# Kernel tuning notes

Hardware: AMD Instinct MI355X
Metric: run time of the kernel (lower is better)

Reference implementation:

```python
import jax, jax.numpy as jnp
import numpy as np

N, E, B = 50000, 800000, 64
ND, ED, HID, NC = 64, 16, 128, 6
HEADS = [4, 4, 1]
CH = [32, 32, 128]
CONCAT = [True, True, False]

PNAMES = ['pW', 'pb'] + [f'{p}{l}' for l in range(3) for p in ['W', 'as', 'ad', 'ae', 'We', 'b', 'g', 'be']] + ['gW1', 'gb1', 'gW2', 'gb2', 'cW1', 'cb1', 'cW2', 'cb2']


def _gat_conv(x, src, dst, ea, W, a_s, a_d, a_e, We, b, heads, ch, concat):
    n = x.shape[0]
    xp = (x @ W).reshape(n, heads, ch)          # [N,H,C]
    al_src = (xp * a_s).sum(-1)                 # [N,H]
    al_dst = (xp * a_d).sum(-1)                 # [N,H]
    ep = (ea @ We).reshape(-1, heads, ch)       # [E,H,C]
    al_edge = (ep * a_e).sum(-1)                # [E,H]
    alpha = jax.nn.leaky_relu(al_src[src] + al_dst[dst] + al_edge, 0.2)
    # segment softmax over destination nodes
    amax = jax.ops.segment_max(alpha, dst, num_segments=n)
    ex = jnp.exp(alpha - amax[dst])
    den = jax.ops.segment_sum(ex, dst, num_segments=n)
    alpha = ex / (den[dst] + 1e-16)
    out = jax.ops.segment_sum(xp[src] * alpha[:, :, None], dst, num_segments=n)
    out = out.reshape(n, heads * ch) if concat else out.mean(axis=1)
    return out + b


def _layernorm(x, g, be):
    m = x.mean(-1, keepdims=True)
    v = ((x - m) ** 2).mean(-1, keepdims=True)
    return (x - m) / jnp.sqrt(v + 1e-5) * g + be


def _forward(x, edge_index, edge_attr, batch, params):
    src, dst = edge_index[0], edge_index[1]
    h = jax.nn.relu(x @ params['pW'] + params['pb'])
    for l in range(3):
        r = h
        h = _gat_conv(h, src, dst, edge_attr, params[f'W{l}'], params[f'as{l}'],
                      params[f'ad{l}'], params[f'ae{l}'], params[f'We{l}'], params[f'b{l}'],
                      HEADS[l], CH[l], CONCAT[l])
        h = _layernorm(h, params[f'g{l}'], params[f'be{l}'])
        h = jax.nn.elu(h)
        h = h + r
    # GlobalAttention pooling: gate MLP + segment softmax over graphs
    gate = jax.nn.relu(h @ params['gW1'] + params['gb1']) @ params['gW2'] + params['gb2']  # [N,1]
    gmax = jax.ops.segment_max(gate, batch, num_segments=B)
    ge = jnp.exp(gate - gmax[batch])
    gden = jax.ops.segment_sum(ge, batch, num_segments=B)
    att = ge / (gden[batch] + 1e-16)
    pooled = jax.ops.segment_sum(att * h, batch, num_segments=B)  # [B,HID]
    return jax.nn.relu(pooled @ params['cW1'] + params['cb1']) @ params['cW2'] + params['cb2']


def setup_inputs() -> dict:
    key = jax.random.key(0)
    ks = iter(jax.random.split(key, 64))
    nx = lambda: next(ks)
    rn = lambda shape, s=0.1: jax.random.normal(nx(), shape, jnp.float32) * s
    inp = {
        'x': jax.random.normal(nx(), (N, ND), jnp.float32),
        'edge_index': jax.random.randint(nx(), (2, E), 0, N),
        'edge_attr': jax.random.normal(nx(), (E, ED), jnp.float32),
        'batch': jnp.sort(jax.random.randint(nx(), (N,), 0, B)),
        'pW': rn((ND, HID)), 'pb': jnp.zeros((HID,), jnp.float32),
    }
    for l in range(3):
        h, c = HEADS[l], CH[l]
        inp[f'W{l}'] = rn((HID, h * c))
        inp[f'as{l}'] = rn((h, c))
        inp[f'ad{l}'] = rn((h, c))
        inp[f'ae{l}'] = rn((h, c))
        inp[f'We{l}'] = rn((ED, h * c))
        inp[f'b{l}'] = jnp.zeros((HID,), jnp.float32)
        inp[f'g{l}'] = jnp.ones((HID,), jnp.float32)
        inp[f'be{l}'] = jnp.zeros((HID,), jnp.float32)
    inp['gW1'] = rn((HID, HID // 2)); inp['gb1'] = jnp.zeros((HID // 2,), jnp.float32)
    inp['gW2'] = rn((HID // 2, 1)); inp['gb2'] = jnp.zeros((1,), jnp.float32)
    inp['cW1'] = rn((HID, HID // 2)); inp['cb1'] = jnp.zeros((HID // 2,), jnp.float32)
    inp['cW2'] = rn((HID // 2, NC)); inp['cb2'] = jnp.zeros((NC,), jnp.float32)
    return inp


def reference(x, edge_index, edge_attr, batch, pW, pb,
              W0, as0, ad0, ae0, We0, b0, g0, be0,
              W1, as1, ad1, ae1, We1, b1, g1, be1,
              W2, as2, ad2, ae2, We2, b2, g2, be2,
              gW1, gb1, gW2, gb2, cW1, cb1, cW2, cb2):
    params = dict(zip(PNAMES, (pW, pb, W0, as0, ad0, ae0, We0, b0, g0, be0,
                               W1, as1, ad1, ae1, We1, b1, g1, be1,
                               W2, as2, ad2, ae2, We2, b2, g2, be2,
                               gW1, gb1, gW2, gb2, cW1, cb1, cW2, cb2)))
    return _forward(x, edge_index, edge_attr, batch, params)
```

## Files before the change

kernel.cpp:

```cpp
#include <hip/hip_runtime.h>
#include <hip/hip_fp16.h>
#include <math.h>

#define N_NODES 50000
#define N_EDGES 800000
#define NB      64
#define ND      64
#define ED      16
#define HID     128
#define NC      6
#define SCAN_BLOCKS ((N_NODES + 255) / 256)
#define GEMM_BLOCKS ((N_NODES + 63) / 64)

typedef _Float16 f16;
typedef f16  half8  __attribute__((ext_vector_type(8)));
typedef float floatx4 __attribute__((ext_vector_type(4)));

__global__ void k_setup(const float* __restrict__ pW, const float* __restrict__ W0,
                        const float* __restrict__ W1, const float* __restrict__ W2,
                        const float* __restrict__ We0, const float* __restrict__ ae0,
                        const float* __restrict__ We1, const float* __restrict__ ae1,
                        const float* __restrict__ We2, const float* __restrict__ ae2,
                        int* __restrict__ deg, float* __restrict__ WeAe,
                        f16* __restrict__ Wtp, f16* __restrict__ Wt0,
                        f16* __restrict__ Wt1, f16* __restrict__ Wt2) {
    int i = blockIdx.x * 256 + threadIdx.x;
    if (i < N_NODES) deg[i] = 0;
    if (i < 128 * 64) {
        int n = i / 64, k = i % 64;
        Wtp[i] = (f16)pW[k * 128 + n];
    }
    if (i < 128 * 128) {
        int n = i / 128, k = i % 128;
        Wt0[i] = (f16)W0[k * 128 + n];
        Wt1[i] = (f16)W1[k * 128 + n];
        Wt2[i] = (f16)W2[k * 128 + n];
    }
    if (i >= 60000 && i < 60144) {
        int t = i - 60000;
        if (t < 64) {
            int k = t >> 2, h = t & 3;
            float s = 0.f;
            for (int c = 0; c < 32; c++) s += We0[k * HID + h * 32 + c] * ae0[h * 32 + c];
            WeAe[k * 9 + h] = s;
        } else if (t < 128) {
            int tt = t - 64;
            int k = tt >> 2, h = tt & 3;
            float s = 0.f;
            for (int c = 0; c < 32; c++) s += We1[k * HID + h * 32 + c] * ae1[h * 32 + c];
            WeAe[k * 9 + 4 + h] = s;
        } else {
            int k = t - 128;
            float s = 0.f;
            for (int c = 0; c < HID; c++) s += We2[k * HID + c] * ae2[c];
            WeAe[k * 9 + 8] = s;
        }
    }
}

template <int K, int MODE>
__global__ __launch_bounds__(256) void k_gemm(
        const float* __restrict__ act, const f16* __restrict__ Wt,
        const float* __restrict__ bias, const float* __restrict__ as_,
        const float* __restrict__ ad_, float* __restrict__ hout,
        __half* __restrict__ xp, float* __restrict__ al_src,
        float* __restrict__ al_dst) {
    constexpr int KP = K + 8;
    __shared__ __align__(16) f16 A[64 * KP];
    __shared__ float part_s[4][64];
    __shared__ float part_d[4][64];
    int tid = threadIdx.x;
    int base = blockIdx.x * 64;

    constexpr int NV = 64 * K / 4 / 256;
    #pragma unroll
    for (int i = 0; i < NV; i++) {
        int v = tid + i * 256;
        int row = v / (K / 4);
        int k4 = v % (K / 4);
        float4 xv = make_float4(0.f, 0.f, 0.f, 0.f);
        if (base + row < N_NODES)
            xv = *(const float4*)(act + (size_t)(base + row) * K + k4 * 4);
        f16* dp = &A[row * KP + k4 * 4];
        dp[0] = (f16)xv.x; dp[1] = (f16)xv.y; dp[2] = (f16)xv.z; dp[3] = (f16)xv.w;
    }
    __syncthreads();

    int w = tid >> 6, l = tid & 63;
    int lm = l & 15, q = l >> 4;
    floatx4 acc[4][2];
    #pragma unroll
    for (int mt = 0; mt < 4; mt++)
        #pragma unroll
        for (int j = 0; j < 2; j++)
            acc[mt][j] = (floatx4){0.f, 0.f, 0.f, 0.f};

    #pragma unroll
    for (int kt = 0; kt < K / 32; kt++) {
        int ko = kt * 32 + q * 8;
        half8 b0 = *(const half8*)(Wt + (size_t)(w * 32 + lm) * K + ko);
        half8 b1 = *(const half8*)(Wt + (size_t)(w * 32 + 16 + lm) * K + ko);
        #pragma unroll
        for (int mt = 0; mt < 4; mt++) {
            half8 a = *(const half8*)(&A[(mt * 16 + lm) * KP + ko]);
            acc[mt][0] = __builtin_amdgcn_mfma_f32_16x16x32_f16(a, b0, acc[mt][0], 0, 0, 0);
            acc[mt][1] = __builtin_amdgcn_mfma_f32_16x16x32_f16(a, b1, acc[mt][1], 0, 0, 0);
        }
    }

    if (MODE == 0) {
        float b0 = bias[w * 32 + lm];
        float b1 = bias[w * 32 + 16 + lm];
        #pragma unroll
        for (int mt = 0; mt < 4; mt++)
            #pragma unroll
            for (int r = 0; r < 4; r++) {
                int row = mt * 16 + q * 4 + r;
                if (base + row < N_NODES) {
                    hout[(size_t)(base + row) * HID + w * 32 + lm]      = fmaxf(acc[mt][0][r] + b0, 0.f);
                    hout[(size_t)(base + row) * HID + w * 32 + 16 + lm] = fmaxf(acc[mt][1][r] + b1, 0.f);
                }
            }
    } else {
        float a0 = as_[w * 32 + lm], a1 = as_[w * 32 + 16 + lm];
        float e0 = ad_[w * 32 + lm], e1 = ad_[w * 32 + 16 + lm];
        float ps[4][4], pd[4][4];
        #pragma unroll
        for (int mt = 0; mt < 4; mt++)
            #pragma unroll
            for (int r = 0; r < 4; r++) {
                ps[mt][r] = acc[mt][0][r] * a0 + acc[mt][1][r] * a1;
                pd[mt][r] = acc[mt][0][r] * e0 + acc[mt][1][r] * e1;
            }
        #pragma unroll
        for (int off = 1; off < 16; off <<= 1)
            #pragma unroll
            for (int mt = 0; mt < 4; mt++)
                #pragma unroll
                for (int r = 0; r < 4; r++) {
                    ps[mt][r] += __shfl_xor(ps[mt][r], off, 64);
                    pd[mt][r] += __shfl_xor(pd[mt][r], off, 64);
                }
        if (MODE == 1) {
            if (lm == 0)
                #pragma unroll
                for (int mt = 0; mt < 4; mt++)
                    #pragma unroll
                    for (int r = 0; r < 4; r++) {
                        int n = base + mt * 16 + q * 4 + r;
                        if (n < N_NODES) {
                            al_src[n * 4 + w] = ps[mt][r];
                            al_dst[n * 4 + w] = pd[mt][r];
                        }
                    }
        } else {
            if (lm == 0)
                #pragma unroll
                for (int mt = 0; mt < 4; mt++)
                    #pragma unroll
                    for (int r = 0; r < 4; r++) {
                        part_s[w][mt * 16 + q * 4 + r] = ps[mt][r];
                        part_d[w][mt * 16 + q * 4 + r] = pd[mt][r];
                    }
        }
        __syncthreads();
        #pragma unroll
        for (int mt = 0; mt < 4; mt++)
            #pragma unroll
            for (int r = 0; r < 4; r++) {
                int row = mt * 16 + q * 4 + r;
                A[row * KP + w * 32 + lm]      = (f16)acc[mt][0][r];
                A[row * KP + w * 32 + 16 + lm] = (f16)acc[mt][1][r];
            }
        if (MODE == 2 && tid < 64) {
            int n = base + tid;
            if (n < N_NODES) {
                al_src[n] = part_s[0][tid] + part_s[1][tid] + part_s[2][tid] + part_s[3][tid];
                al_dst[n] = part_d[0][tid] + part_d[1][tid] + part_d[2][tid] + part_d[3][tid];
            }
        }
        __syncthreads();
        #pragma unroll
        for (int i = 0; i < 4; i++) {
            int v = tid + i * 256;
            int row = v >> 4, c8 = v & 15;
            if (base + row < N_NODES) {
                float4 hv = *(const float4*)(&A[row * KP + c8 * 8]);
                *reinterpret_cast<float4*>(reinterpret_cast<char*>(xp) +
                    ((size_t)(base + row) * HID + c8 * 8) * 2) = hv;
            }
        }
    }
}

__global__ void k_deg(const int* __restrict__ dst, int* __restrict__ deg,
                      int* __restrict__ rank) {
    int e = blockIdx.x * blockDim.x + threadIdx.x;
    if (e < N_EDGES) rank[e] = atomicAdd(&deg[dst[e]], 1);
}

__global__ void k_scanA(const int* __restrict__ deg, int* __restrict__ bsum) {
    __shared__ int wsu[4];
    int t = threadIdx.x;
    int i = blockIdx.x * 256 + t;
    int d = (i < N_NODES) ? deg[i] : 0;
    int v = d;
    #pragma unroll
    for (int o = 32; o > 0; o >>= 1) v += __shfl_xor(v, o, 64);
    if ((t & 63) == 0) wsu[t >> 6] = v;
    __syncthreads();
    if (t == 0) bsum[blockIdx.x] = wsu[0] + wsu[1] + wsu[2] + wsu[3];
}

__global__ void k_scanB(const int* __restrict__ bsum, int* __restrict__ bpre,
                        int* __restrict__ offs) {
    __shared__ int sc[256];
    int t = threadIdx.x;
    int d = (t < SCAN_BLOCKS) ? bsum[t] : 0;
    sc[t] = d;
    __syncthreads();
    for (int o = 1; o < 256; o <<= 1) {
        int v = (t >= o) ? sc[t - o] : 0;
        __syncthreads();
        sc[t] += v;
        __syncthreads();
    }
    if (t < SCAN_BLOCKS) bpre[t] = sc[t] - d;
    if (t == 0) offs[N_NODES] = N_EDGES;
}

__global__ void k_scanC(const int* __restrict__ deg, const int* __restrict__ bpre,
                        int* __restrict__ offs) {
    __shared__ int sc[256];
    int t = threadIdx.x;
    int i = blockIdx.x * 256 + t;
    int d = (i < N_NODES) ? deg[i] : 0;
    sc[t] = d;
    __syncthreads();
    for (int o = 1; o < 256; o <<= 1) {
        int v = (t >= o) ? sc[t - o] : 0;
        __syncthreads();
        sc[t] += v;
        __syncthreads();
    }
    if (i < N_NODES) offs[i] = bpre[blockIdx.x] + sc[t] - d;
}

__global__ void k_edge_build(const int* __restrict__ src, const int* __restrict__ dst,
                             const int* __restrict__ rank, const int* __restrict__ offs,
                             const float* __restrict__ ea, const float* __restrict__ WeAe,
                             float4* __restrict__ rec) {
    __shared__ float w[ED * 9];
    __shared__ float4 rs[256][4];
    __shared__ int rp[256];
    int tid = threadIdx.x;
    if (tid < ED * 9) w[tid] = WeAe[tid];
    __syncthreads();
    int e = blockIdx.x * 256 + tid;
    if (e < N_EDGES) {
        float ev[ED];
        const float4* ep4 = reinterpret_cast<const float4*>(ea + (size_t)e * ED);
        #pragma unroll
        for (int q = 0; q < 4; q++) {
            float4 v = ep4[q];
            ev[q * 4 + 0] = v.x; ev[q * 4 + 1] = v.y;
            ev[q * 4 + 2] = v.z; ev[q * 4 + 3] = v.w;
        }
        float r[9];
        #pragma unroll
        for (int j = 0; j < 9; j++) r[j] = 0.f;
        #pragma unroll
        for (int k = 0; k < ED; k++) {
            float evk = ev[k];
            #pragma unroll
            for (int j = 0; j < 9; j++) r[j] += evk * w[k * 9 + j];
        }
        int d = dst[e], s = src[e];
        rp[tid] = offs[d] + rank[e];
        rs[tid][0] = make_float4(r[0], r[1], r[2], r[3]);
        rs[tid][1] = make_float4(r[4], r[5], r[6], r[7]);
        rs[tid][2] = make_float4(r[8], __int_as_float(s), __int_as_float(d), 0.f);
        rs[tid][3] = make_float4(0.f, 0.f, 0.f, 0.f);
    } else {
        rp[tid] = -1;
    }
    __syncthreads();
    int g0 = tid >> 2, q = tid & 3;
    #pragma unroll
    for (int rr = 0; rr < 4; rr++) {
        int g = rr * 64 + g0;
        int p = rp[g];
        if (p >= 0) rec[(size_t)p * 4 + q] = rs[g][q];
    }
}

template <int H, int SLOT>
__global__ void k_node_agg(const int* __restrict__ offs, const float4* __restrict__ rec,
                           const float* __restrict__ al_src, const float* __restrict__ al_dst,
                           const __half* __restrict__ xp, const float* __restrict__ bias,
                           const float* __restrict__ g, const float* __restrict__ be,
                           const float* __restrict__ hin, float* __restrict__ hout) {
    int tid = threadIdx.x;
    int wave = tid >> 6;
    int lane = tid & 63;
    int n = blockIdx.x * 4 + wave;
    if (n >= N_NODES) return;
    int e0 = offs[n], e1 = offs[n + 1];
    int side = lane >> 4;
    int cl = lane & 15;
    int c = cl * 8;
    int h = cl >> 2;
    float ald = (H == 4) ? al_dst[n * 4 + h] : al_dst[n];
    float acc[8] = {0.f, 0.f, 0.f, 0.f, 0.f, 0.f, 0.f, 0.f};
    float den = 0.f;

    auto fetchw = [&](int i, int& s, float& wv) {
        if (i < e1) {
            const float* rb = (const float*)(rec + (size_t)i * 4);
            s = __float_as_int(rb[9]);
            float r = (H == 4) ? rb[SLOT * 4 + h] : rb[8];
            float al = ((H == 4) ? al_src[s * 4 + h] : al_src[s]) + ald + r;
            al = (al >= 0.f) ? al : 0.2f * al;
            wv = __expf(al);
        } else { s = 0; wv = 0.f; }
    };
    auto accum = [&](uint4 r, float wv) {
        union { uint4 u; __half2 h2[4]; } t2; t2.u = r;
        #pragma unroll
        for (int j = 0; j < 4; j++) {
            float2 f = __half22float2(t2.h2[j]);
            acc[j * 2]     += wv * f.x;
            acc[j * 2 + 1] += wv * f.y;
        }
        den += wv;
    };

    int i = e0 + side;
    int sA, sB; float wA, wB;
    fetchw(i, sA, wA);
    fetchw(i + 4, sB, wB);
    while (i < e1) {
        uint4 rA = *reinterpret_cast<const uint4*>(xp + (size_t)sA * HID + c);
        uint4 rB = *reinterpret_cast<const uint4*>(xp + (size_t)sB * HID + c);
        int sC, sD; float wC, wD;
        fetchw(i + 8, sC, wC);
        fetchw(i + 12, sD, wD);
        accum(rA, wA);
        accum(rB, wB);
        sA = sC; wA = wC; sB = sD; wB = wD;
        i += 8;
    }
    #pragma unroll
    for (int j = 0; j < 8; j++) {
        acc[j] += __shfl_xor(acc[j], 16, 64);
        acc[j] += __shfl_xor(acc[j], 32, 64);
    }
    den += __shfl_xor(den, 16, 64);
    den += __shfl_xor(den, 32, 64);

    float inv = 1.f / (den + 1e-16f);
    float v[8];
    const float4 bv0 = *reinterpret_cast<const float4*>(bias + c);
    const float4 bv1 = *reinterpret_cast<const float4*>(bias + c + 4);
    v[0] = acc[0] * inv + bv0.x; v[1] = acc[1] * inv + bv0.y;
    v[2] = acc[2] * inv + bv0.z; v[3] = acc[3] * inv + bv0.w;
    v[4] = acc[4] * inv + bv1.x; v[5] = acc[5] * inv + bv1.y;
    v[6] = acc[6] * inv + bv1.z; v[7] = acc[7] * inv + bv1.w;
    float s8 = v[0] + v[1] + v[2] + v[3] + v[4] + v[5] + v[6] + v[7];
    #pragma unroll
    for (int o = 8; o > 0; o >>= 1) s8 += __shfl_xor(s8, o, 64);
    float mean = s8 * (1.f / HID);
    float q8 = 0.f;
    float d[8];
    #pragma unroll
    for (int j = 0; j < 8; j++) { d[j] = v[j] - mean; q8 += d[j] * d[j]; }
    #pragma unroll
    for (int o = 8; o > 0; o >>= 1) q8 += __shfl_xor(q8, o, 64);
    float rstd = rsqrtf(q8 * (1.f / HID) + 1e-5f);
    if (side < 2) {
        int co = c + side * 4;
        int j0 = side * 4;
        const float4 gv  = *reinterpret_cast<const float4*>(g + co);
        const float4 bev = *reinterpret_cast<const float4*>(be + co);
        float y0 = d[j0]     * rstd * gv.x + bev.x;
        float y1 = d[j0 + 1] * rstd * gv.y + bev.y;
        float y2 = d[j0 + 2] * rstd * gv.z + bev.z;
        float y3 = d[j0 + 3] * rstd * gv.w + bev.w;
        y0 = (y0 > 0.f) ? y0 : (__expf(y0) - 1.f);
        y1 = (y1 > 0.f) ? y1 : (__expf(y1) - 1.f);
        y2 = (y2 > 0.f) ? y2 : (__expf(y2) - 1.f);
        y3 = (y3 > 0.f) ? y3 : (__expf(y3) - 1.f);
        const float4 rv = *reinterpret_cast<const float4*>(hin + (size_t)n * HID + co);
        *reinterpret_cast<float4*>(hout + (size_t)n * HID + co) =
            make_float4(y0 + rv.x, y1 + rv.y, y2 + rv.z, y3 + rv.w);
    }
}

__global__ void k_gate(const float* __restrict__ h, const float* __restrict__ gW1,
                       const float* __restrict__ gb1, const float* __restrict__ gW2,
                       const float* __restrict__ gb2, const int* __restrict__ batch,
                       float* __restrict__ gate, int* __restrict__ goff) {
    __shared__ float hs[16][HID];
    int tid = threadIdx.x;
    int base = blockIdx.x * 16;
    if (tid < 16) {
        int n = base + tid;
        int cur = batch[n];
        int prev = (n == 0) ? -1 : batch[n - 1];
        for (int gg = prev + 1; gg <= cur; gg++) goff[gg] = n;
        if (n == N_NODES - 1)
            for (int gg = cur + 1; gg <= NB; gg++) goff[gg] = N_NODES;
    }
    for (int idx = tid; idx < 16 * HID; idx += 256) {
        int nn = idx >> 7, k = idx & 127;
        hs[nn][k] = h[(size_t)(base + nn) * HID + k];
    }
    __syncthreads();
    int c = tid & 63;
    int wave = tid >> 6;
    float acc[4] = {0.f, 0.f, 0.f, 0.f};
    #pragma unroll 8
    for (int k = 0; k < HID; k++) {
        float wv = gW1[k * 64 + c];
        #pragma unroll
        for (int q = 0; q < 4; q++) acc[q] += hs[wave * 4 + q][k] * wv;
    }
    float b1 = gb1[c], w2 = gW2[c];
    float p[4];
    #pragma unroll
    for (int q = 0; q < 4; q++) p[q] = fmaxf(acc[q] + b1, 0.f) * w2;
    #pragma unroll
    for (int o = 32; o > 0; o >>= 1) {
        #pragma unroll
        for (int q = 0; q < 4; q++) p[q] += __shfl_xor(p[q], o, 64);
    }
    if (c == 0) {
        float b2 = gb2[0];
        #pragma unroll
        for (int q = 0; q < 4; q++) gate[base + wave * 4 + q] = p[q] + b2;
    }
}

__global__ void k_pool_head(const float* __restrict__ h, const float* __restrict__ gate,
                            const int* __restrict__ goff, const float* __restrict__ cW1,
                            const float* __restrict__ cb1, const float* __restrict__ cW2,
                            const float* __restrict__ cb2, float* __restrict__ out) {
    __shared__ float red[256];
    __shared__ float tr[64];
    int b = blockIdx.x;
    int t = threadIdx.x;
    int sG = goff[b], eG = goff[b + 1];
    float m = -__builtin_inff();
    for (int n = sG + t; n < eG; n += 256) m = fmaxf(m, gate[n]);
    red[t] = m;
    __syncthreads();
    for (int o = 128; o > 0; o >>= 1) { if (t < o) red[t] = fmaxf(red[t], red[t + o]); __syncthreads(); }
    m = red[0];
    __syncthreads();
    float dd = 0.f;
    for (int n = sG + t; n < eG; n += 256) dd += __expf(gate[n] - m);
    red[t] = dd;
    __syncthreads();
    for (int o = 128; o > 0; o >>= 1) { if (t < o) red[t] += red[t + o]; __syncthreads(); }
    float dinv = 1.f / (red[0] + 1e-16f);
    __syncthreads();
    int c = t & 127, pg = t >> 7;
    float acc = 0.f;
    for (int n = sG + pg; n < eG; n += 2)
        acc += __expf(gate[n] - m) * h[(size_t)n * HID + c];
    acc *= dinv;
    red[t] = acc;
    __syncthreads();
    float pc = 0.f;
    if (t < 128) pc = red[t] + red[t + 128];
    __syncthreads();
    if (t < 128) red[t] = pc;
    __syncthreads();
    if (t < 64) {
        float a = cb1[t];
        #pragma unroll 8
        for (int k = 0; k < HID; k++) a += red[k] * cW1[k * 64 + t];
        tr[t] = fmaxf(a, 0.f);
    }
    __syncthreads();
    if (t < NC) {
        float o = cb2[t];
        #pragma unroll
        for (int k = 0; k < 64; k++) o += tr[k] * cW2[k * NC + t];
        out[b * NC + t] = o;
    }
}

extern "C" void kernel_launch(void* const* d_in, const int* in_sizes, int n_in,
                              void* d_out, int out_size, void* d_ws, size_t ws_size,
                              hipStream_t stream) {
    (void)in_sizes; (void)n_in; (void)out_size; (void)ws_size;
    const float* x     = (const float*)d_in[0];
    const int*   ei    = (const int*)d_in[1];
    const float* ea    = (const float*)d_in[2];
    const int*   batch = (const int*)d_in[3];
    const float* pW    = (const float*)d_in[4];
    const float* pb    = (const float*)d_in[5];
    const float *W[3], *as_[3], *ad_[3], *ae_[3], *We[3], *bb[3], *gg[3], *be[3];
    for (int l = 0; l < 3; l++) {
        int base = 6 + 8 * l;
        W[l]   = (const float*)d_in[base + 0];
        as_[l] = (const float*)d_in[base + 1];
        ad_[l] = (const float*)d_in[base + 2];
        ae_[l] = (const float*)d_in[base + 3];
        We[l]  = (const float*)d_in[base + 4];
        bb[l]  = (const float*)d_in[base + 5];
        gg[l]  = (const float*)d_in[base + 6];
        be[l]  = (const float*)d_in[base + 7];
    }
    const float* gW1 = (const float*)d_in[30];
    const float* gb1 = (const float*)d_in[31];
    const float* gW2 = (const float*)d_in[32];
    const float* gb2 = (const float*)d_in[33];
    const float* cW1 = (const float*)d_in[34];
    const float* cb1 = (const float*)d_in[35];
    const float* cW2 = (const float*)d_in[36];
    const float* cb2 = (const float*)d_in[37];
    float* out = (float*)d_out;

    char* p = (char*)d_ws;
    auto take = [&](size_t bytes) -> char* {
        char* r = p;
        p += (bytes + 255) & ~(size_t)255;
        return r;
    };
    float*  h0      = (float*)take((size_t)N_NODES * HID * 4);
    float*  h1      = (float*)take((size_t)N_NODES * HID * 4);
    __half* xp      = (__half*)take((size_t)N_NODES * HID * 2);
    float*  al_src  = (float*)take((size_t)N_NODES * 4 * 4);
    float*  al_dst  = (float*)take((size_t)N_NODES * 4 * 4);
    float4* rec     = (float4*)take((size_t)N_EDGES * 64);
    int*    deg     = (int*)take((size_t)N_NODES * 4);
    int*    offs    = (int*)take((size_t)(N_NODES + 1) * 4);
    int*    rank    = (int*)take((size_t)N_EDGES * 4);
    int*    bsum    = (int*)take(256 * 4);
    int*    bpre    = (int*)take(256 * 4);
    float*  WeAe    = (float*)take(ED * 9 * 4);
    float*  gate    = (float*)take((size_t)N_NODES * 4);
    int*    goff    = (int*)take((NB + 1) * 4);
    f16*    Wtp     = (f16*)take(128 * 64 * 2);
    f16*    Wt0     = (f16*)take(128 * 128 * 2);
    f16*    Wt1     = (f16*)take(128 * 128 * 2);
    f16*    Wt2     = (f16*)take(128 * 128 * 2);
    f16*    Wt[3]   = {Wt0, Wt1, Wt2};

    const int* src = ei;
    const int* dst = ei + N_EDGES;

    k_setup<<<256, 256, 0, stream>>>(pW, W[0], W[1], W[2], We[0], ae_[0], We[1], ae_[1],
                                     We[2], ae_[2], deg, WeAe, Wtp, Wt0, Wt1, Wt2);
    k_gemm<64, 0><<<GEMM_BLOCKS, 256, 0, stream>>>(x, Wtp, pb, nullptr, nullptr,
                                                   h0, nullptr, nullptr, nullptr);
    k_deg<<<(N_EDGES + 255) / 256, 256, 0, stream>>>(dst, deg, rank);
    k_scanA<<<SCAN_BLOCKS, 256, 0, stream>>>(deg, bsum);
    k_scanB<<<1, 256, 0, stream>>>(bsum, bpre, offs);
    k_scanC<<<SCAN_BLOCKS, 256, 0, stream>>>(deg, bpre, offs);
    k_edge_build<<<(N_EDGES + 255) / 256, 256, 0, stream>>>(src, dst, rank, offs, ea, WeAe, rec);

    float* hc = h0;
    float* hn = h1;
    k_gemm<128, 1><<<GEMM_BLOCKS, 256, 0, stream>>>(hc, Wt[0], nullptr, as_[0], ad_[0],
                                                    nullptr, xp, al_src, al_dst);
    k_node_agg<4, 0><<<(N_NODES + 3) / 4, 256, 0, stream>>>(offs, rec, al_src, al_dst, xp,
                                                            bb[0], gg[0], be[0], hc, hn);
    { float* t = hc; hc = hn; hn = t; }
    k_gemm<128, 1><<<GEMM_BLOCKS, 256, 0, stream>>>(hc, Wt[1], nullptr, as_[1], ad_[1],
                                                    nullptr, xp, al_src, al_dst);
    k_node_agg<4, 1><<<(N_NODES + 3) / 4, 256, 0, stream>>>(offs, rec, al_src, al_dst, xp,
                                                            bb[1], gg[1], be[1], hc, hn);
    { float* t = hc; hc = hn; hn = t; }
    k_gemm<128, 2><<<GEMM_BLOCKS, 256, 0, stream>>>(hc, Wt[2], nullptr, as_[2], ad_[2],
                                                    nullptr, xp, al_src, al_dst);
    k_node_agg<1, 0><<<(N_NODES + 3) / 4, 256, 0, stream>>>(offs, rec, al_src, al_dst, xp,
                                                            bb[2], gg[2], be[2], hc, hn);
    { float* t = hc; hc = hn; hn = t; }

    k_gate<<<N_NODES / 16, 256, 0, stream>>>(hc, gW1, gb1, gW2, gb2, batch, gate, goff);
    k_pool_head<<<NB, 256, 0, stream>>>(hc, gate, goff, cW1, cb1, cW2, cb2, out);
}
```

Measured before the change: 579.3 us.

## Split pooling across graph-parallel blocks with atomic accumulation and separate head

Replaces the single 64-block pool+classifier kernel with three kernels: one computes per-graph softmax max and denominator, one spreads the weighted feature sum over NB x 32 blocks and combines partials with atomicAdd, and one runs the classifier MLP. The old kernel launched only 64 blocks, each walking roughly 780 nodes serially, which left most of the GPU idle. The new version adds two kernel launches, float atomics (so summation order is no longer deterministic), and a zeroing of the pooled buffer in the setup kernel.

New measurement: 494.9 us. 1.17x faster.

```diff
diff --git a/kernel.cpp b/kernel.cpp
--- a/kernel.cpp
+++ b/kernel.cpp
@@ -9,6 +9,7 @@
 #define ED      16
 #define HID     128
 #define NC      6
+#define POOL_SPLIT 32
 #define SCAN_BLOCKS ((N_NODES + 255) / 256)
 #define GEMM_BLOCKS ((N_NODES + 63) / 64)
 
@@ -21,11 +22,13 @@
                         const float* __restrict__ We0, const float* __restrict__ ae0,
                         const float* __restrict__ We1, const float* __restrict__ ae1,
                         const float* __restrict__ We2, const float* __restrict__ ae2,
-                        int* __restrict__ deg, float* __restrict__ WeAe,
+                        int* __restrict__ deg, float* __restrict__ pooled,
+                        float* __restrict__ WeAe,
                         f16* __restrict__ Wtp, f16* __restrict__ Wt0,
                         f16* __restrict__ Wt1, f16* __restrict__ Wt2) {
     int i = blockIdx.x * 256 + threadIdx.x;
     if (i < N_NODES) deg[i] = 0;
+    if (i < NB * HID) pooled[i] = 0.f;
     if (i < 128 * 64) {
         int n = i / 64, k = i % 64;
         Wtp[i] = (f16)pW[k * 128 + n];
@@ -441,47 +444,58 @@
     }
 }
 
-__global__ void k_pool_head(const float* __restrict__ h, const float* __restrict__ gate,
-                            const int* __restrict__ goff, const float* __restrict__ cW1,
-                            const float* __restrict__ cb1, const float* __restrict__ cW2,
-                            const float* __restrict__ cb2, float* __restrict__ out) {
-    __shared__ float red[256];
-    __shared__ float tr[64];
+__global__ void k_gmaxden(const float* __restrict__ gate, const int* __restrict__ goff,
+                          float* __restrict__ gmax, float* __restrict__ gden) {
     int b = blockIdx.x;
     int t = threadIdx.x;
-    int sG = goff[b], eG = goff[b + 1];
+    __shared__ float red[256];
+    int s = goff[b], e = goff[b + 1];
     float m = -__builtin_inff();
-    for (int n = sG + t; n < eG; n += 256) m = fmaxf(m, gate[n]);
+    for (int n = s + t; n < e; n += 256) m = fmaxf(m, gate[n]);
     red[t] = m;
     __syncthreads();
     for (int o = 128; o > 0; o >>= 1) { if (t < o) red[t] = fmaxf(red[t], red[t + o]); __syncthreads(); }
     m = red[0];
     __syncthreads();
-    float dd = 0.f;
-    for (int n = sG + t; n < eG; n += 256) dd += __expf(gate[n] - m);
-    red[t] = dd;
+    float d = 0.f;
+    for (int n = s + t; n < e; n += 256) d += __expf(gate[n] - m);
+    red[t] = d;
     __syncthreads();
     for (int o = 128; o > 0; o >>= 1) { if (t < o) red[t] += red[t + o]; __syncthreads(); }
-    float dinv = 1.f / (red[0] + 1e-16f);
-    __syncthreads();
-    int c = t & 127, pg = t >> 7;
+    if (t == 0) { gmax[b] = m; gden[b] = red[0]; }
+}
+
+__global__ void k_pool(const float* __restrict__ h, const float* __restrict__ gate,
+                       const float* __restrict__ gmax, const float* __restrict__ gden,
+                       const int* __restrict__ goff, float* __restrict__ pooled) {
+    int b = blockIdx.x;
+    int part = blockIdx.y;
+    int c = threadIdx.x;
+    int s = goff[b], e = goff[b + 1];
+    float m = gmax[b];
+    float dinv = 1.f / (gden[b] + 1e-16f);
     float acc = 0.f;
-    for (int n = sG + pg; n < eG; n += 2)
-        acc += __expf(gate[n] - m) * h[(size_t)n * HID + c];
-    acc *= dinv;
-    red[t] = acc;
-    __syncthreads();
-    float pc = 0.f;
-    if (t < 128) pc = red[t] + red[t + 128];
-    __syncthreads();
-    if (t < 128) red[t] = pc;
-    __syncthreads();
-    if (t < 64) {
-        float a = cb1[t];
-        #pragma unroll 8
-        for (int k = 0; k < HID; k++) a += red[k] * cW1[k * 64 + t];
-        tr[t] = fmaxf(a, 0.f);
-    }
+    for (int n = s + part; n < e; n += POOL_SPLIT) {
+        float att = __expf(gate[n] - m) * dinv;
+        acc += att * h[(size_t)n * HID + c];
+    }
+    atomicAdd(&pooled[b * HID + c], acc);
+}
+
+__global__ void k_head(const float* __restrict__ pooled, const float* __restrict__ cW1,
+                       const float* __restrict__ cb1, const float* __restrict__ cW2,
+                       const float* __restrict__ cb2, float* __restrict__ out) {
+    int b = blockIdx.x;
+    int t = threadIdx.x;
+    __shared__ float pr[HID];
+    __shared__ float tr[64];
+    pr[t] = pooled[b * HID + t];
+    pr[t + 64] = pooled[b * HID + t + 64];
+    __syncthreads();
+    float a = cb1[t];
+    #pragma unroll 8
+    for (int k = 0; k < HID; k++) a += pr[k] * cW1[k * 64 + t];
+    tr[t] = fmaxf(a, 0.f);
     __syncthreads();
     if (t < NC) {
         float o = cb2[t];
@@ -542,7 +556,10 @@
     int*    bpre    = (int*)take(256 * 4);
     float*  WeAe    = (float*)take(ED * 9 * 4);
     float*  gate    = (float*)take((size_t)N_NODES * 4);
+    float*  gmax    = (float*)take(NB * 4);
+    float*  gden    = (float*)take(NB * 4);
     int*    goff    = (int*)take((NB + 1) * 4);
+    float*  pooled  = (float*)take(NB * HID * 4);
     f16*    Wtp     = (f16*)take(128 * 64 * 2);
     f16*    Wt0     = (f16*)take(128 * 128 * 2);
     f16*    Wt1     = (f16*)take(128 * 128 * 2);
@@ -553,7 +570,7 @@
     const int* dst = ei + N_EDGES;
 
     k_setup<<<256, 256, 0, stream>>>(pW, W[0], W[1], W[2], We[0], ae_[0], We[1], ae_[1],
-                                     We[2], ae_[2], deg, WeAe, Wtp, Wt0, Wt1, Wt2);
+                                     We[2], ae_[2], deg, pooled, WeAe, Wtp, Wt0, Wt1, Wt2);
     k_gemm<64, 0><<<GEMM_BLOCKS, 256, 0, stream>>>(x, Wtp, pb, nullptr, nullptr,
                                                    h0, nullptr, nullptr, nullptr);
     k_deg<<<(N_EDGES + 255) / 256, 256, 0, stream>>>(dst, deg, rank);
@@ -581,5 +598,7 @@
     { float* t = hc; hc = hn; hn = t; }
 
     k_gate<<<N_NODES / 16, 256, 0, stream>>>(hc, gW1, gb1, gW2, gb2, batch, gate, goff);
-    k_pool_head<<<NB, 256, 0, stream>>>(hc, gate, goff, cW1, cb1, cW2, cb2, out);
-}
+    k_gmaxden<<<NB, 256, 0, stream>>>(gate, goff, gmax, gden);
+    k_pool<<<dim3(NB, POOL_SPLIT), HID, 0, stream>>>(hc, gate, gmax, gden, goff, pooled);
+    k_head<<<NB, 64, 0, stream>>>(pooled, cW1, cb1, cW2, cb2, out);
+}
```
